# Kernel optimization log

Hardware: AMD Instinct MI355X
Metric: run time of the kernel (lower is better)

The kernel has to match this reference:

```python
import jax, jax.numpy as jnp
import numpy as np
from jax.ops import segment_sum

N_NODES = 10000
N_EDGES = 320000


def leaky_relu(x):
    return jnp.where(x >= 0, x, 0.01 * x)


def gcn_layer(edge_h, src, dst, W, b):
    # (1) node h = mean of incoming edge features
    deg = segment_sum(jnp.ones((edge_h.shape[0],), edge_h.dtype), dst, num_segments=N_NODES)
    deg = jnp.maximum(deg, 1.0)
    h = segment_sum(edge_h, dst, num_segments=N_NODES) / deg[:, None]
    # (2) update_all: node h = sum over in-edges of src node h
    h2 = segment_sum(h[src], dst, num_segments=N_NODES)
    # (3) edge h = mean of endpoint node features
    eh = 0.5 * (h2[src] + h2[dst])
    # (4) linear on edge features
    return eh @ W.T + b


def setup_inputs() -> dict:
    key = jax.random.key(0)
    ks = jax.random.split(key, 20)
    d_in, d_h, d_out = 128, 256, 64
    inp = {
        'inputs1': jax.random.normal(ks[0], (N_EDGES, d_in), jnp.float32),
        'src1': jax.random.randint(ks[1], (N_EDGES,), 0, N_NODES, jnp.int32),
        'dst1': jax.random.randint(ks[2], (N_EDGES,), 0, N_NODES, jnp.int32),
        'inputs2': jax.random.normal(ks[3], (N_EDGES, d_in), jnp.float32),
        'src2': jax.random.randint(ks[4], (N_EDGES,), 0, N_NODES, jnp.int32),
        'dst2': jax.random.randint(ks[5], (N_EDGES,), 0, N_NODES, jnp.int32),
        'W11': jax.random.normal(ks[6], (d_h, d_in), jnp.float32) * 0.05,
        'b11': jax.random.normal(ks[7], (d_h,), jnp.float32) * 0.05,
        'W12': jax.random.normal(ks[8], (d_h, d_h), jnp.float32) * 0.05,
        'b12': jax.random.normal(ks[9], (d_h,), jnp.float32) * 0.05,
        'W21': jax.random.normal(ks[10], (d_h, d_in), jnp.float32) * 0.05,
        'b21': jax.random.normal(ks[11], (d_h,), jnp.float32) * 0.05,
        'W22': jax.random.normal(ks[12], (d_h, d_h), jnp.float32) * 0.05,
        'b22': jax.random.normal(ks[13], (d_h,), jnp.float32) * 0.05,
        'W3': jax.random.normal(ks[14], (d_out, 2 * d_h), jnp.float32) * 0.05,
        'b3': jax.random.normal(ks[15], (d_out,), jnp.float32) * 0.05,
    }
    return inp


def reference(inputs1, src1, dst1, inputs2, src2, dst2,
              W11, b11, W12, b12, W21, b21, W22, b22, W3, b3):
    h1 = leaky_relu(gcn_layer(inputs1, src1, dst1, W11, b11))
    h1 = leaky_relu(gcn_layer(h1, src1, dst1, W12, b12))
    h1 = jnp.mean(h1, axis=0)
    h2 = leaky_relu(gcn_layer(inputs2, src2, dst2, W21, b21))
    h2 = leaky_relu(gcn_layer(h2, src2, dst2, W22, b22))
    h2 = jnp.mean(h2, axis=0)
    out = jnp.concatenate((h1, h2), axis=0)
    return out @ W3.T + b3
```

## Files before the change

### kernel.cpp

```cpp
#include <hip/hip_runtime.h>
#include <cstddef>

#define NN 10000
#define NB 2500

typedef unsigned int u32;
typedef unsigned short u16;
typedef __attribute__((ext_vector_type(8))) short short8;
typedef __attribute__((ext_vector_type(4))) float f32x4;

__device__ __forceinline__ float lrelu(float x) { return x >= 0.f ? x : 0.01f * x; }

__device__ __forceinline__ float bf_lo(u32 v) { union { u32 i; float f; } c; c.i = v << 16; return c.f; }
__device__ __forceinline__ float bf_hi(u32 v) { union { u32 i; float f; } c; c.i = v & 0xFFFF0000u; return c.f; }
__device__ __forceinline__ u32 rne_bits(float f) {
  union { float f; u32 i; } c; c.f = f;
  return c.i + 0x7FFFu + ((c.i >> 16) & 1u);
}
__device__ __forceinline__ u32 pack2(float a, float b) {
  return (rne_bits(a) >> 16) | (rne_bits(b) & 0xFFFF0000u);
}

__global__ __launch_bounds__(256) void wconv_kernel(
    const float* __restrict__ a, const float* __restrict__ b,
    const float* __restrict__ c, const float* __restrict__ d,
    u16* __restrict__ oa, u16* __restrict__ ob,
    u16* __restrict__ oc, u16* __restrict__ od,
    int* __restrict__ degbase ) {
  int i = blockIdx.x * 256 + threadIdx.x;
  if (i < 32768) oa[i] = (u16)(rne_bits(a[i]) >> 16);
  else if (i < 98304) ob[i - 32768] = (u16)(rne_bits(b[i - 32768]) >> 16);
  else if (i < 131072) oc[i - 98304] = (u16)(rne_bits(c[i - 98304]) >> 16);
  else if (i < 196608) od[i - 131072] = (u16)(rne_bits(d[i - 131072]) >> 16);
  if (i < 4 * NN) degbase[i] = 0;
}

__global__ __launch_bounds__(256) void count_b_kernel(const int* __restrict__ dstA,
                                                      const int* __restrict__ dstB,
                                                      int* __restrict__ degbase, int E) {
  const int g = blockIdx.y;
  const int* dst = g ? dstB : dstA;
  int* degi = degbase + (size_t)g * 2 * NN;
  int e = blockIdx.x * 256 + threadIdx.x;
  if (e < E) atomicAdd(&degi[dst[e]], 1);
}

__global__ __launch_bounds__(1024) void scan_b_kernel(const int* __restrict__ degbase,
                                                      int* __restrict__ offbase,
                                                      float* __restrict__ rdegbase, int n) {
  const int g = blockIdx.x;
  const int* degi = degbase + (size_t)g * 2 * NN;
  int* off = offbase + (size_t)g * NN;
  float* rdeg = rdegbase + (size_t)g * NN;
  __shared__ int wsum[16];
  __shared__ int wpre[16];
  __shared__ int carry_s;
  const int tid = threadIdx.x;
  const int lane = tid & 63, w = tid >> 6;
  if (tid == 0) carry_s = 0;
  __syncthreads();
  for (int base = 0; base < n; base += 1024) {
    int i = base + tid;
    int x = (i < n) ? degi[i] : 0;
    int v = x;
#pragma unroll
    for (int d = 1; d < 64; d <<= 1) {
      int t = __shfl_up(v, d);
      if (lane >= d) v += t;
    }
    if (lane == 63) wsum[w] = v;
    __syncthreads();
    if (tid == 0) {
      int s = carry_s;
#pragma unroll
      for (int j = 0; j < 16; ++j) { int t = wsum[j]; wpre[j] = s; s += t; }
      carry_s = s;
    }
    __syncthreads();
    if (i < n) {
      off[i] = wpre[w] + (v - x);
      rdeg[i] = 1.0f / fmaxf((float)x, 1.0f);
    }
    __syncthreads();
  }
}

__global__ __launch_bounds__(256) void fill_b_kernel(const int* __restrict__ srcA,
                                                     const int* __restrict__ dstA,
                                                     const int* __restrict__ srcB,
                                                     const int* __restrict__ dstB,
                                                     const int* __restrict__ offbase,
                                                     int* __restrict__ degbase,
                                                     int* __restrict__ eid_sb,
                                                     int* __restrict__ esrc_sb, int E) {
  const int g = blockIdx.y;
  const int* src = g ? srcB : srcA;
  const int* dst = g ? dstB : dstA;
  const int* off = offbase + (size_t)g * NN;
  int* cursor = degbase + (size_t)g * 2 * NN + NN;
  int* eid_s = eid_sb + (size_t)g * E;
  int* esrc_s = esrc_sb + (size_t)g * E;
  int e = blockIdx.x * 256 + threadIdx.x;
  if (e < E) {
    int d = dst[e];
    int p = off[d] + atomicAdd(&cursor[d], 1);
    eid_s[p] = e;
    esrc_s[p] = src[e];
  }
}

__global__ __launch_bounds__(256) void gatherA_b_kernel(
    const float* __restrict__ featA, const float* __restrict__ featB,
    const int* __restrict__ gidxb, const int* __restrict__ offbase,
    const int* __restrict__ degbase, const float* __restrict__ rdegbase,
    u32* __restrict__ outbfb , int E) {
  const int g = blockIdx.y;
  const float* feat = g ? featB : featA;
  const int* gidx = gidxb + (size_t)g * E;
  const int* off = offbase + (size_t)g * NN;
  const int* degi = degbase + (size_t)g * 2 * NN;
  const float* rdeg = rdegbase + (size_t)g * NN;
  u32* outbf = outbfb + (size_t)g * NN * 64;
  const int n = (blockIdx.x << 2) + (threadIdx.x >> 6);
  const int lane = threadIdx.x & 63;
  const int hl = lane & 31, h = lane >> 5;
  const int o = off[n], d = degi[n];
  const int fo = hl << 2;
  float4 acc = make_float4(0.f, 0.f, 0.f, 0.f);
  for (int c0 = 0; c0 < d; c0 += 64) {
    const int m = min(64, d - c0);
    const int gg = (lane < m) ? gidx[o + c0 + lane] : 0;
    const int pairs = m >> 1;
    int i = 0;
    for (; i + 4 <= pairs; i += 4) {
      const int e0 = 2 * i + h;
      const int s0 = __shfl(gg, e0), s1 = __shfl(gg, e0 + 2);
      const int s2 = __shfl(gg, e0 + 4), s3 = __shfl(gg, e0 + 6);
      const float4 v0 = *(const float4*)&feat[(s0 << 7) + fo];
      const float4 v1 = *(const float4*)&feat[(s1 << 7) + fo];
      const float4 v2 = *(const float4*)&feat[(s2 << 7) + fo];
      const float4 v3 = *(const float4*)&feat[(s3 << 7) + fo];
      acc.x += (v0.x + v1.x) + (v2.x + v3.x);
      acc.y += (v0.y + v1.y) + (v2.y + v3.y);
      acc.z += (v0.z + v1.z) + (v2.z + v3.z);
      acc.w += (v0.w + v1.w) + (v2.w + v3.w);
    }
    for (; i < pairs; ++i) {
      const int s0 = __shfl(gg, 2 * i + h);
      const float4 v0 = *(const float4*)&feat[(s0 << 7) + fo];
      acc.x += v0.x; acc.y += v0.y; acc.z += v0.z; acc.w += v0.w;
    }
    if (m & 1) {
      const int s0 = __shfl(gg, m - 1);
      const float wgt = (h == 0) ? 1.f : 0.f;
      const float4 v0 = *(const float4*)&feat[(s0 << 7) + fo];
      acc.x = fmaf(v0.x, wgt, acc.x);
      acc.y = fmaf(v0.y, wgt, acc.y);
      acc.z = fmaf(v0.z, wgt, acc.z);
      acc.w = fmaf(v0.w, wgt, acc.w);
    }
  }
  acc.x += __shfl(acc.x, lane ^ 32);
  acc.y += __shfl(acc.y, lane ^ 32);
  acc.z += __shfl(acc.z, lane ^ 32);
  acc.w += __shfl(acc.w, lane ^ 32);
  if (h == 0) {
    const float sc = rdeg[n];
    uint2 r;
    r.x = pack2(acc.x * sc, acc.y * sc);
    r.y = pack2(acc.z * sc, acc.w * sc);
    *(uint2*)&outbf[(size_t)n * 64 + (hl << 1)] = r;
  }
}

__global__ __launch_bounds__(256) void gatherB_b_kernel(
    const u32* __restrict__ featb , const int* __restrict__ gidxb,
    const int* __restrict__ offbase, const int* __restrict__ degbase,
    u32* __restrict__ outbfb, int E) {
  const int bid = blockIdx.x;
  const int r = bid & 7, t = bid >> 3;
  const int g = r >> 2;
  const int nb = t * 4 + (r & 3);
  const u32* feat = featb + (size_t)g * NN * 64;
  const int* gidx = gidxb + (size_t)g * E;
  const int* off = offbase + (size_t)g * NN;
  const int* degi = degbase + (size_t)g * 2 * NN;
  u32* outbf = outbfb + (size_t)g * NN * 64;
  const int n = (nb << 2) + (threadIdx.x >> 6);
  const int lane = threadIdx.x & 63;
  const int hl = lane & 31, h = lane >> 5;
  const int o = off[n], d = degi[n];
  const int fo = hl << 1;
  float4 acc = make_float4(0.f, 0.f, 0.f, 0.f);
  for (int c0 = 0; c0 < d; c0 += 64) {
    const int m = min(64, d - c0);
    const int gg = (lane < m) ? gidx[o + c0 + lane] : 0;
    const int pairs = m >> 1;
    int i = 0;
    for (; i + 4 <= pairs; i += 4) {
      const int e0 = 2 * i + h;
      const int s0 = __shfl(gg, e0), s1 = __shfl(gg, e0 + 2);
      const int s2 = __shfl(gg, e0 + 4), s3 = __shfl(gg, e0 + 6);
      const uint2 v0 = *(const uint2*)&feat[(s0 << 6) + fo];
      const uint2 v1 = *(const uint2*)&feat[(s1 << 6) + fo];
      const uint2 v2 = *(const uint2*)&feat[(s2 << 6) + fo];
      const uint2 v3 = *(const uint2*)&feat[(s3 << 6) + fo];
      acc.x += (bf_lo(v0.x) + bf_lo(v1.x)) + (bf_lo(v2.x) + bf_lo(v3.x));
      acc.y += (bf_hi(v0.x) + bf_hi(v1.x)) + (bf_hi(v2.x) + bf_hi(v3.x));
      acc.z += (bf_lo(v0.y) + bf_lo(v1.y)) + (bf_lo(v2.y) + bf_lo(v3.y));
      acc.w += (bf_hi(v0.y) + bf_hi(v1.y)) + (bf_hi(v2.y) + bf_hi(v3.y));
    }
    for (; i < pairs; ++i) {
      const int s0 = __shfl(gg, 2 * i + h);
      const uint2 v0 = *(const uint2*)&feat[(s0 << 6) + fo];
      acc.x += bf_lo(v0.x); acc.y += bf_hi(v0.x);
      acc.z += bf_lo(v0.y); acc.w += bf_hi(v0.y);
    }
    if (m & 1) {
      const int s0 = __shfl(gg, m - 1);
      const float wgt = (h == 0) ? 1.f : 0.f;
      const uint2 v0 = *(const uint2*)&feat[(s0 << 6) + fo];
      acc.x = fmaf(bf_lo(v0.x), wgt, acc.x);
      acc.y = fmaf(bf_hi(v0.x), wgt, acc.y);
      acc.z = fmaf(bf_lo(v0.y), wgt, acc.z);
      acc.w = fmaf(bf_hi(v0.y), wgt, acc.w);
    }
  }
  acc.x += __shfl(acc.x, lane ^ 32);
  acc.y += __shfl(acc.y, lane ^ 32);
  acc.z += __shfl(acc.z, lane ^ 32);
  acc.w += __shfl(acc.w, lane ^ 32);
  if (h == 0) {
    uint2 r2;
    r2.x = pack2(acc.x, acc.y);
    r2.y = pack2(acc.z, acc.w);
    *(uint2*)&outbf[(size_t)n * 64 + (hl << 1)] = r2;
  }
}

__device__ __forceinline__ void acc_bf4(float4& a, uint2 v, const float4& zn, const float4& bb) {
  a.x += lrelu(0.5f * (bf_lo(v.x) + zn.x) + bb.x);
  a.y += lrelu(0.5f * (bf_hi(v.x) + zn.y) + bb.y);
  a.z += lrelu(0.5f * (bf_lo(v.y) + zn.z) + bb.z);
  a.w += lrelu(0.5f * (bf_hi(v.y) + zn.w) + bb.w);
}

__global__ __launch_bounds__(256) void passC_b_kernel(
    const u32* __restrict__ Zb_, const int* __restrict__ esrcb,
    const int* __restrict__ offbase, const int* __restrict__ degbase,
    const float* __restrict__ rdegbase,
    const float* __restrict__ biasA, const float* __restrict__ biasB,
    u32* __restrict__ hBb, int E) {
  const int bid = blockIdx.x;
  const int r = bid & 7, t = bid >> 3;
  const int g = r >> 2, fh = (r >> 1) & 1;
  const int nb = t * 2 + (r & 1);
  const u32* Z = Zb_ + (size_t)g * NN * 128;
  const int* esrc = esrcb + (size_t)g * E;
  const int* off = offbase + (size_t)g * NN;
  const int* degi = degbase + (size_t)g * 2 * NN;
  const float* rdeg = rdegbase + (size_t)g * NN;
  const float* bias = g ? biasB : biasA;
  u32* hB = hBb + (size_t)g * NN * 128;
  const int n = (nb << 2) + (threadIdx.x >> 6);
  const int lane = threadIdx.x & 63;
  const int hl = lane & 31, h = lane >> 5;
  const int o = off[n], d = degi[n];
  const int fo = (fh << 6) + (hl << 1);
  const uint2 znv = *(const uint2*)&Z[(n << 7) + fo];
  const float4 zn = make_float4(bf_lo(znv.x), bf_hi(znv.x), bf_lo(znv.y), bf_hi(znv.y));
  const float4 bb = *(const float4*)&bias[(fh << 7) + (hl << 2)];
  float4 a = make_float4(0.f, 0.f, 0.f, 0.f);
  for (int c0 = 0; c0 < d; c0 += 64) {
    const int m = min(64, d - c0);
    const int gg = (lane < m) ? esrc[o + c0 + lane] : 0;
    const int pairs = m >> 1;
    int i = 0;
    for (; i + 4 <= pairs; i += 4) {
      const int e0 = 2 * i + h;
      const int s0 = __shfl(gg, e0), s1 = __shfl(gg, e0 + 2);
      const int s2 = __shfl(gg, e0 + 4), s3 = __shfl(gg, e0 + 6);
      const uint2 z0 = *(const uint2*)&Z[(s0 << 7) + fo];
      const uint2 z1 = *(const uint2*)&Z[(s1 << 7) + fo];
      const uint2 z2 = *(const uint2*)&Z[(s2 << 7) + fo];
      const uint2 z3 = *(const uint2*)&Z[(s3 << 7) + fo];
      acc_bf4(a, z0, zn, bb);
      acc_bf4(a, z1, zn, bb);
      acc_bf4(a, z2, zn, bb);
      acc_bf4(a, z3, zn, bb);
    }
    for (; i < pairs; ++i) {
      const int s0 = __shfl(gg, 2 * i + h);
      const uint2 z0 = *(const uint2*)&Z[(s0 << 7) + fo];
      acc_bf4(a, z0, zn, bb);
    }
    if (m & 1) {
      const int s0 = __shfl(gg, m - 1);
      const uint2 z0 = *(const uint2*)&Z[(s0 << 7) + fo];
      if (h == 0) acc_bf4(a, z0, zn, bb);
    }
  }
  a.x += __shfl(a.x, lane ^ 32); a.y += __shfl(a.y, lane ^ 32);
  a.z += __shfl(a.z, lane ^ 32); a.w += __shfl(a.w, lane ^ 32);
  if (h == 0) {
    const float rr = rdeg[n];
    uint2 outv;
    outv.x = pack2(a.x * rr, a.y * rr);
    outv.y = pack2(a.z * rr, a.w * rr);
    *(uint2*)&hB[(n << 7) + fo] = outv;
  }
}

__global__ __launch_bounds__(256) void gatherC_b_kernel(
    const u32* __restrict__ featb , const int* __restrict__ gidxb,
    const int* __restrict__ offbase, const int* __restrict__ degbase,
    u32* __restrict__ outbfb, int E) {
  const int bid = blockIdx.x;
  const int r = bid & 7, t = bid >> 3;
  const int g = r >> 2, fh = (r >> 1) & 1;
  const int nb = t * 2 + (r & 1);
  const u32* feat = featb + (size_t)g * NN * 128;
  const int* gidx = gidxb + (size_t)g * E;
  const int* off = offbase + (size_t)g * NN;
  const int* degi = degbase + (size_t)g * 2 * NN;
  u32* outbf = outbfb + (size_t)g * NN * 128;
  const int n = (nb << 2) + (threadIdx.x >> 6);
  const int lane = threadIdx.x & 63;
  const int hl = lane & 31, h = lane >> 5;
  const int o = off[n], d = degi[n];
  const int fo = (fh << 6) + (hl << 1);
  float4 a = make_float4(0.f, 0.f, 0.f, 0.f);
  for (int c0 = 0; c0 < d; c0 += 64) {
    const int m = min(64, d - c0);
    const int gg = (lane < m) ? gidx[o + c0 + lane] : 0;
    const int pairs = m >> 1;
    int i = 0;
    for (; i + 4 <= pairs; i += 4) {
      const int e0 = 2 * i + h;
      const int s0 = __shfl(gg, e0), s1 = __shfl(gg, e0 + 2);
      const int s2 = __shfl(gg, e0 + 4), s3 = __shfl(gg, e0 + 6);
      const uint2 z0 = *(const uint2*)&feat[(s0 << 7) + fo];
      const uint2 z1 = *(const uint2*)&feat[(s1 << 7) + fo];
      const uint2 z2 = *(const uint2*)&feat[(s2 << 7) + fo];
      const uint2 z3 = *(const uint2*)&feat[(s3 << 7) + fo];
      a.x += (bf_lo(z0.x) + bf_lo(z1.x)) + (bf_lo(z2.x) + bf_lo(z3.x));
      a.y += (bf_hi(z0.x) + bf_hi(z1.x)) + (bf_hi(z2.x) + bf_hi(z3.x));
      a.z += (bf_lo(z0.y) + bf_lo(z1.y)) + (bf_lo(z2.y) + bf_lo(z3.y));
      a.w += (bf_hi(z0.y) + bf_hi(z1.y)) + (bf_hi(z2.y) + bf_hi(z3.y));
    }
    for (; i < pairs; ++i) {
      const int s0 = __shfl(gg, 2 * i + h);
      const uint2 z0 = *(const uint2*)&feat[(s0 << 7) + fo];
      a.x += bf_lo(z0.x); a.y += bf_hi(z0.x);
      a.z += bf_lo(z0.y); a.w += bf_hi(z0.y);
    }
    if (m & 1) {
      const int s0 = __shfl(gg, m - 1);
      const uint2 z0 = *(const uint2*)&feat[(s0 << 7) + fo];
      if (h == 0) {
        a.x += bf_lo(z0.x); a.y += bf_hi(z0.x);
        a.z += bf_lo(z0.y); a.w += bf_hi(z0.y);
      }
    }
  }
  a.x += __shfl(a.x, lane ^ 32); a.y += __shfl(a.y, lane ^ 32);
  a.z += __shfl(a.z, lane ^ 32); a.w += __shfl(a.w, lane ^ 32);
  if (h == 0) {
    uint2 outv;
    outv.x = pack2(a.x, a.y);
    outv.y = pack2(a.z, a.w);
    *(uint2*)&outbf[(n << 7) + fo] = outv;
  }
}

__global__ __launch_bounds__(256) void passE_b_kernel(
    const u32* __restrict__ Z2b, const int* __restrict__ esrcb,
    const int* __restrict__ offbase, const int* __restrict__ degbase,
    const float* __restrict__ biasA, const float* __restrict__ biasB,
    float* __restrict__ partialsb , int nNodes, int E) {
  const int bid = blockIdx.x;
  const int r = bid & 7, t = bid >> 3;
  const int g = r >> 2, fh = (r >> 1) & 1;
  const int blk = t * 2 + (r & 1);
  const u32* Z2 = Z2b + (size_t)g * NN * 128;
  const int* esrc = esrcb + (size_t)g * E;
  const int* off = offbase + (size_t)g * NN;
  const int* degi = degbase + (size_t)g * 2 * NN;
  const float* bias = g ? biasB : biasA;
  float* partials = partialsb + (size_t)((g * 2 + fh) * 128 + blk) * 128;
  const int lane = threadIdx.x & 63, w = threadIdx.x >> 6;
  const int hl = lane & 31, h = lane >> 5;
  const int fo = (fh << 6) + (hl << 1);
  const float4 bb = *(const float4*)&bias[(fh << 7) + (hl << 2)];
  float4 a = make_float4(0.f, 0.f, 0.f, 0.f);
  for (int n = blk * 4 + w; n < nNodes; n += 512) {
    const int o = off[n], d = degi[n];
    const uint2 znv = *(const uint2*)&Z2[(n << 7) + fo];
    const float4 zn = make_float4(bf_lo(znv.x), bf_hi(znv.x), bf_lo(znv.y), bf_hi(znv.y));
    for (int c0 = 0; c0 < d; c0 += 64) {
      const int m = min(64, d - c0);
      const int gg = (lane < m) ? esrc[o + c0 + lane] : 0;
      const int pairs = m >> 1;
      int i = 0;
      for (; i + 4 <= pairs; i += 4) {
        const int e0 = 2 * i + h;
        const int s0 = __shfl(gg, e0), s1 = __shfl(gg, e0 + 2);
        const int s2 = __shfl(gg, e0 + 4), s3 = __shfl(gg, e0 + 6);
        const uint2 z0 = *(const uint2*)&Z2[(s0 << 7) + fo];
        const uint2 z1 = *(const uint2*)&Z2[(s1 << 7) + fo];
        const uint2 z2 = *(const uint2*)&Z2[(s2 << 7) + fo];
        const uint2 z3 = *(const uint2*)&Z2[(s3 << 7) + fo];
        acc_bf4(a, z0, zn, bb);
        acc_bf4(a, z1, zn, bb);
        acc_bf4(a, z2, zn, bb);
        acc_bf4(a, z3, zn, bb);
      }
      for (; i < pairs; ++i) {
        const int s0 = __shfl(gg, 2 * i + h);
        const uint2 z0 = *(const uint2*)&Z2[(s0 << 7) + fo];
        acc_bf4(a, z0, zn, bb);
      }
      if (m & 1) {
        const int s0 = __shfl(gg, m - 1);
        const uint2 z0 = *(const uint2*)&Z2[(s0 << 7) + fo];
        if (h == 0) acc_bf4(a, z0, zn, bb);
      }
    }
  }
  a.x += __shfl(a.x, lane ^ 32); a.y += __shfl(a.y, lane ^ 32);
  a.z += __shfl(a.z, lane ^ 32); a.w += __shfl(a.w, lane ^ 32);
  __shared__ float red[4][128];
  if (h == 0) *(float4*)&red[w][hl << 2] = a;
  __syncthreads();
  const int tid = threadIdx.x;
  if (tid < 128) partials[tid] = red[0][tid] + red[1][tid] + red[2][tid] + red[3][tid];
}

__global__ __launch_bounds__(1024) void final_fused_kernel(
    const float* __restrict__ partialsb ,
    const float* __restrict__ W3, const float* __restrict__ b3,
    float* __restrict__ out, float invE) {
  __shared__ float smacc[512];
  __shared__ float tmp2[2][512];
  __shared__ float red[16][64];
  const int tid = threadIdx.x;
  {
    const int half = tid >> 9;
    const int q = tid & 511;
    const float* basep = partialsb + (size_t)(q >> 7) * 128 * 128 + (q & 127);
    float s = 0.f;
    for (int b = half * 64; b < half * 64 + 64; ++b) s += basep[(size_t)b * 128];
    tmp2[half][q] = s;
  }
  __syncthreads();
  if (tid < 512) smacc[tid] = tmp2[0][tid] + tmp2[1][tid];
  __syncthreads();
  const int j = tid & 63, part = tid >> 6;
  float acc = 0.f;
  for (int kk = 0; kk < 32; ++kk) {
    const int k = part * 32 + kk;
    acc += smacc[k] * W3[(size_t)j * 512 + k];
  }
  red[part][j] = acc;
  __syncthreads();
  if (part == 0) {
    float s = 0.f;
#pragma unroll
    for (int p = 0; p < 16; ++p) s += red[p][j];
    out[j] = b3[j] + s * invE;
  }
}

template <int K>
__global__ __launch_bounds__(256) void gemm_mfma_b_kernel(const u16* __restrict__ Ab,
                                                          const u16* __restrict__ WA,
                                                          const u16* __restrict__ WB,
                                                          u16* __restrict__ Cb, int N) {
  const int g = blockIdx.z;
  const u16* A = Ab + (size_t)g * NN * K;
  const u16* Wb = g ? WB : WA;
  u16* C = Cb + (size_t)g * NN * 256;
  const int lane = threadIdx.x & 63;
  const int w = threadIdx.x >> 6;
  const int wm = w >> 1, wn = w & 1;
  const int bn = blockIdx.x * 64 + wm * 32;
  const int bo = blockIdx.y * 64 + wn * 32;
  const int r0 = lane & 15;
  const int kq = lane >> 4;
  const int ra0 = min(bn + r0, N - 1);
  const int ra1 = min(bn + 16 + r0, N - 1);
  const u16* a0p = &A[(size_t)ra0 * K + kq * 8];
  const u16* a1p = &A[(size_t)ra1 * K + kq * 8];
  const u16* b0p = &Wb[(size_t)(bo + r0) * K + kq * 8];
  const u16* b1p = &Wb[(size_t)(bo + 16 + r0) * K + kq * 8];
  f32x4 acc00 = {0.f, 0.f, 0.f, 0.f}, acc01 = {0.f, 0.f, 0.f, 0.f};
  f32x4 acc10 = {0.f, 0.f, 0.f, 0.f}, acc11 = {0.f, 0.f, 0.f, 0.f};
#pragma unroll
  for (int k0 = 0; k0 < K; k0 += 32) {
    const short8 a0 = *(const short8*)(a0p + k0);
    const short8 a1 = *(const short8*)(a1p + k0);
    const short8 b0 = *(const short8*)(b0p + k0);
    const short8 b1 = *(const short8*)(b1p + k0);
    acc00 = __builtin_amdgcn_mfma_f32_16x16x32_bf16(a0, b0, acc00, 0, 0, 0);
    acc01 = __builtin_amdgcn_mfma_f32_16x16x32_bf16(a0, b1, acc01, 0, 0, 0);
    acc10 = __builtin_amdgcn_mfma_f32_16x16x32_bf16(a1, b0, acc10, 0, 0, 0);
    acc11 = __builtin_amdgcn_mfma_f32_16x16x32_bf16(a1, b1, acc11, 0, 0, 0);
  }
#pragma unroll
  for (int r = 0; r < 4; ++r) {
    const int n0 = bn + 4 * kq + r;
    if (n0 < N) {
      C[(size_t)n0 * 256 + bo + r0] = (u16)(rne_bits(acc00[r]) >> 16);
      C[(size_t)n0 * 256 + bo + 16 + r0] = (u16)(rne_bits(acc01[r]) >> 16);
    }
    const int n1 = bn + 16 + 4 * kq + r;
    if (n1 < N) {
      C[(size_t)n1 * 256 + bo + r0] = (u16)(rne_bits(acc10[r]) >> 16);
      C[(size_t)n1 * 256 + bo + 16 + r0] = (u16)(rne_bits(acc11[r]) >> 16);
    }
  }
}

extern "C" void kernel_launch(void* const* d_in, const int* in_sizes, int n_in,
                              void* d_out, int out_size, void* d_ws, size_t ws_size,
                              hipStream_t stream) {
  const float* in1 = (const float*)d_in[0];
  const int* src1 = (const int*)d_in[1];
  const int* dst1 = (const int*)d_in[2];
  const float* in2 = (const float*)d_in[3];
  const int* src2 = (const int*)d_in[4];
  const int* dst2 = (const int*)d_in[5];
  const float* W11 = (const float*)d_in[6];
  const float* b11 = (const float*)d_in[7];
  const float* W12 = (const float*)d_in[8];
  const float* b12 = (const float*)d_in[9];
  const float* W21 = (const float*)d_in[10];
  const float* b21 = (const float*)d_in[11];
  const float* W22 = (const float*)d_in[12];
  const float* b22 = (const float*)d_in[13];
  const float* W3 = (const float*)d_in[14];
  const float* b3 = (const float*)d_in[15];
  const int E = in_sizes[1];
  const int N = NN;

  char* base = (char*)d_ws;
  size_t pos = 0;
  auto carve = [&](size_t bytes) -> char* {
    char* p = base + pos;
    pos = (pos + bytes + 511) & ~(size_t)511;
    return p;
  };
  int* degbase = (int*)carve((size_t)2 * 2 * N * sizeof(int));
  int* offb = (int*)carve((size_t)2 * N * sizeof(int));
  float* rdegb = (float*)carve((size_t)2 * N * sizeof(float));
  int* eid_sb = (int*)carve((size_t)2 * E * sizeof(int));
  int* esrc_sb = (int*)carve((size_t)2 * E * sizeof(int));
  u32* Hb = (u32*)carve((size_t)2 * N * 64 * sizeof(u32));
  u32* H2b = (u32*)carve((size_t)2 * N * 64 * sizeof(u32));
  u32* Zb = (u32*)carve((size_t)2 * N * 128 * sizeof(u32));
  u32* HBb = (u32*)carve((size_t)2 * N * 128 * sizeof(u32));
  u32* H2Bb = (u32*)carve((size_t)2 * N * 128 * sizeof(u32));
  u16* Wa1 = (u16*)carve((size_t)32768 * sizeof(u16));
  u16* Wb1 = (u16*)carve((size_t)65536 * sizeof(u16));
  u16* Wa2 = (u16*)carve((size_t)32768 * sizeof(u16));
  u16* Wb2 = (u16*)carve((size_t)65536 * sizeof(u16));
  float* partialsb = (float*)carve((size_t)2 * 2 * 128 * 128 * sizeof(float));
  (void)ws_size; (void)n_in; (void)out_size;

  const int EB = (E + 255) / 256;
  const dim3 g2(EB, 2);
  const dim3 n2(NB, 2);
  const dim3 gemm_grid((N + 63) / 64, 4, 2);

  wconv_kernel<<<768, 256, 0, stream>>>(W11, W12, W21, W22, Wa1, Wb1, Wa2, Wb2, degbase);

  count_b_kernel<<<g2, 256, 0, stream>>>(dst1, dst2, degbase, E);
  scan_b_kernel<<<2, 1024, 0, stream>>>(degbase, offb, rdegb, N);
  fill_b_kernel<<<g2, 256, 0, stream>>>(src1, dst1, src2, dst2, offb, degbase, eid_sb, esrc_sb, E);

  gatherA_b_kernel<<<n2, 256, 0, stream>>>(in1, in2, eid_sb, offb, degbase, rdegb, Hb, E);
  gatherB_b_kernel<<<2 * NB, 256, 0, stream>>>(Hb, esrc_sb, offb, degbase, H2b, E);
  gemm_mfma_b_kernel<128><<<gemm_grid, 256, 0, stream>>>((const u16*)H2b, Wa1, Wa2, (u16*)Zb, N);

  passC_b_kernel<<<4 * NB, 256, 0, stream>>>(Zb, esrc_sb, offb, degbase, rdegb, b11, b21, HBb, E);
  gatherC_b_kernel<<<4 * NB, 256, 0, stream>>>(HBb, esrc_sb, offb, degbase, H2Bb, E);
  gemm_mfma_b_kernel<256><<<gemm_grid, 256, 0, stream>>>((const u16*)H2Bb, Wb1, Wb2, (u16*)Zb, N);

  passE_b_kernel<<<512, 256, 0, stream>>>(Zb, esrc_sb, offb, degbase, b12, b22, partialsb, N, E);
  final_fused_kernel<<<1, 1024, 0, stream>>>(partialsb, W3, b3, (float*)d_out, 1.0f / (float)E);
}
```

Before: 353.4 us.

## Widen gather loads to 16-byte per lane with quarter-wave edge split

Restructures the four edge-gather kernels so each wavefront splits into four 16-lane groups that each load 8 bf16 features (uint4) per neighbor, instead of two 32-lane halves loading 4 features (uint2). Fewer, wider memory transactions per edge and fewer shuffles per edge-batch are the aim, at the cost of a two-stage cross-lane reduction and more accumulator registers. The leaky-ReLU epilogue is also simplified to fma plus fmax, with the node term and bias precomputed once per node.

Result: faster. 329.7 us (-6.7%).

```diff
diff --git a/kernel.cpp b/kernel.cpp
--- a/kernel.cpp
+++ b/kernel.cpp
@@ -8,8 +8,6 @@
 typedef unsigned short u16;
 typedef __attribute__((ext_vector_type(8))) short short8;
 typedef __attribute__((ext_vector_type(4))) float f32x4;
-
-__device__ __forceinline__ float lrelu(float x) { return x >= 0.f ? x : 0.01f * x; }
 
 __device__ __forceinline__ float bf_lo(u32 v) { union { u32 i; float f; } c; c.i = v << 16; return c.f; }
 __device__ __forceinline__ float bf_hi(u32 v) { union { u32 i; float f; } c; c.i = v & 0xFFFF0000u; return c.f; }
@@ -20,6 +18,7 @@
 __device__ __forceinline__ u32 pack2(float a, float b) {
   return (rne_bits(a) >> 16) | (rne_bits(b) & 0xFFFF0000u);
 }
+__device__ __forceinline__ float lrmax(float x) { return fmaxf(x, 0.01f * x); }
 
 __global__ __launch_bounds__(256) void wconv_kernel(
     const float* __restrict__ a, const float* __restrict__ b,
@@ -173,6 +172,16 @@
   }
 }
 
+#define QREDUCE8(aL, aH)                                                   \
+  aL.x += __shfl(aL.x, lane ^ 16); aL.y += __shfl(aL.y, lane ^ 16);        \
+  aL.z += __shfl(aL.z, lane ^ 16); aL.w += __shfl(aL.w, lane ^ 16);        \
+  aH.x += __shfl(aH.x, lane ^ 16); aH.y += __shfl(aH.y, lane ^ 16);        \
+  aH.z += __shfl(aH.z, lane ^ 16); aH.w += __shfl(aH.w, lane ^ 16);        \
+  aL.x += __shfl(aL.x, lane ^ 32); aL.y += __shfl(aL.y, lane ^ 32);        \
+  aL.z += __shfl(aL.z, lane ^ 32); aL.w += __shfl(aL.w, lane ^ 32);        \
+  aH.x += __shfl(aH.x, lane ^ 32); aH.y += __shfl(aH.y, lane ^ 32);        \
+  aH.z += __shfl(aH.z, lane ^ 32); aH.w += __shfl(aH.w, lane ^ 32);
+
 __global__ __launch_bounds__(256) void gatherB_b_kernel(
     const u32* __restrict__ featb , const int* __restrict__ gidxb,
     const int* __restrict__ offbase, const int* __restrict__ degbase,
@@ -188,61 +197,78 @@
   u32* outbf = outbfb + (size_t)g * NN * 64;
   const int n = (nb << 2) + (threadIdx.x >> 6);
   const int lane = threadIdx.x & 63;
-  const int hl = lane & 31, h = lane >> 5;
+  const int q = lane >> 4, ql = lane & 15;
   const int o = off[n], d = degi[n];
-  const int fo = hl << 1;
-  float4 acc = make_float4(0.f, 0.f, 0.f, 0.f);
+  const int fo = ql << 2;
+  float4 aL = make_float4(0.f, 0.f, 0.f, 0.f), aH = make_float4(0.f, 0.f, 0.f, 0.f);
   for (int c0 = 0; c0 < d; c0 += 64) {
     const int m = min(64, d - c0);
     const int gg = (lane < m) ? gidx[o + c0 + lane] : 0;
-    const int pairs = m >> 1;
+    const int full = m >> 2;
     int i = 0;
-    for (; i + 4 <= pairs; i += 4) {
-      const int e0 = 2 * i + h;
-      const int s0 = __shfl(gg, e0), s1 = __shfl(gg, e0 + 2);
-      const int s2 = __shfl(gg, e0 + 4), s3 = __shfl(gg, e0 + 6);
-      const uint2 v0 = *(const uint2*)&feat[(s0 << 6) + fo];
-      const uint2 v1 = *(const uint2*)&feat[(s1 << 6) + fo];
-      const uint2 v2 = *(const uint2*)&feat[(s2 << 6) + fo];
-      const uint2 v3 = *(const uint2*)&feat[(s3 << 6) + fo];
-      acc.x += (bf_lo(v0.x) + bf_lo(v1.x)) + (bf_lo(v2.x) + bf_lo(v3.x));
-      acc.y += (bf_hi(v0.x) + bf_hi(v1.x)) + (bf_hi(v2.x) + bf_hi(v3.x));
-      acc.z += (bf_lo(v0.y) + bf_lo(v1.y)) + (bf_lo(v2.y) + bf_lo(v3.y));
-      acc.w += (bf_hi(v0.y) + bf_hi(v1.y)) + (bf_hi(v2.y) + bf_hi(v3.y));
-    }
-    for (; i < pairs; ++i) {
-      const int s0 = __shfl(gg, 2 * i + h);
-      const uint2 v0 = *(const uint2*)&feat[(s0 << 6) + fo];
-      acc.x += bf_lo(v0.x); acc.y += bf_hi(v0.x);
-      acc.z += bf_lo(v0.y); acc.w += bf_hi(v0.y);
-    }
-    if (m & 1) {
-      const int s0 = __shfl(gg, m - 1);
-      const float wgt = (h == 0) ? 1.f : 0.f;
-      const uint2 v0 = *(const uint2*)&feat[(s0 << 6) + fo];
-      acc.x = fmaf(bf_lo(v0.x), wgt, acc.x);
-      acc.y = fmaf(bf_hi(v0.x), wgt, acc.y);
-      acc.z = fmaf(bf_lo(v0.y), wgt, acc.z);
-      acc.w = fmaf(bf_hi(v0.y), wgt, acc.w);
-    }
-  }
-  acc.x += __shfl(acc.x, lane ^ 32);
-  acc.y += __shfl(acc.y, lane ^ 32);
-  acc.z += __shfl(acc.z, lane ^ 32);
-  acc.w += __shfl(acc.w, lane ^ 32);
-  if (h == 0) {
-    uint2 r2;
-    r2.x = pack2(acc.x, acc.y);
-    r2.y = pack2(acc.z, acc.w);
-    *(uint2*)&outbf[(size_t)n * 64 + (hl << 1)] = r2;
-  }
-}
-
-__device__ __forceinline__ void acc_bf4(float4& a, uint2 v, const float4& zn, const float4& bb) {
-  a.x += lrelu(0.5f * (bf_lo(v.x) + zn.x) + bb.x);
-  a.y += lrelu(0.5f * (bf_hi(v.x) + zn.y) + bb.y);
-  a.z += lrelu(0.5f * (bf_lo(v.y) + zn.z) + bb.z);
-  a.w += lrelu(0.5f * (bf_hi(v.y) + zn.w) + bb.w);
+    for (; i + 2 <= full; i += 2) {
+      const int e0 = 4 * i + q;
+      const int s0 = __shfl(gg, e0), s1 = __shfl(gg, e0 + 4);
+      const uint4 v0 = *(const uint4*)&feat[(s0 << 6) + fo];
+      const uint4 v1 = *(const uint4*)&feat[(s1 << 6) + fo];
+      aL.x += bf_lo(v0.x) + bf_lo(v1.x); aL.y += bf_hi(v0.x) + bf_hi(v1.x);
+      aL.z += bf_lo(v0.y) + bf_lo(v1.y); aL.w += bf_hi(v0.y) + bf_hi(v1.y);
+      aH.x += bf_lo(v0.z) + bf_lo(v1.z); aH.y += bf_hi(v0.z) + bf_hi(v1.z);
+      aH.z += bf_lo(v0.w) + bf_lo(v1.w); aH.w += bf_hi(v0.w) + bf_hi(v1.w);
+    }
+    if (i < full) {
+      const int s0 = __shfl(gg, 4 * i + q);
+      const uint4 v0 = *(const uint4*)&feat[(s0 << 6) + fo];
+      aL.x += bf_lo(v0.x); aL.y += bf_hi(v0.x);
+      aL.z += bf_lo(v0.y); aL.w += bf_hi(v0.y);
+      aH.x += bf_lo(v0.z); aH.y += bf_hi(v0.z);
+      aH.z += bf_lo(v0.w); aH.w += bf_hi(v0.w);
+    }
+    if (m & 3) {
+      const int e = (m & ~3) + q;
+      const int s0 = __shfl(gg, e < m ? e : (m - 1));
+      const float wgt = (e < m) ? 1.f : 0.f;
+      const uint4 v0 = *(const uint4*)&feat[(s0 << 6) + fo];
+      aL.x = fmaf(bf_lo(v0.x), wgt, aL.x); aL.y = fmaf(bf_hi(v0.x), wgt, aL.y);
+      aL.z = fmaf(bf_lo(v0.y), wgt, aL.z); aL.w = fmaf(bf_hi(v0.y), wgt, aL.w);
+      aH.x = fmaf(bf_lo(v0.z), wgt, aH.x); aH.y = fmaf(bf_hi(v0.z), wgt, aH.y);
+      aH.z = fmaf(bf_lo(v0.w), wgt, aH.z); aH.w = fmaf(bf_hi(v0.w), wgt, aH.w);
+    }
+  }
+  QREDUCE8(aL, aH)
+  if (lane < 16) {
+    uint4 outv;
+    outv.x = pack2(aL.x, aL.y);
+    outv.y = pack2(aL.z, aL.w);
+    outv.z = pack2(aH.x, aH.y);
+    outv.w = pack2(aH.z, aH.w);
+    *(uint4*)&outbf[(n << 6) + fo] = outv;
+  }
+}
+
+__device__ __forceinline__ void acc_lr8(float4& aL, float4& aH, uint4 v,
+                                        const float4& wL, const float4& wH) {
+  float u;
+  u = fmaf(bf_lo(v.x), 0.5f, wL.x); aL.x += lrmax(u);
+  u = fmaf(bf_hi(v.x), 0.5f, wL.y); aL.y += lrmax(u);
+  u = fmaf(bf_lo(v.y), 0.5f, wL.z); aL.z += lrmax(u);
+  u = fmaf(bf_hi(v.y), 0.5f, wL.w); aL.w += lrmax(u);
+  u = fmaf(bf_lo(v.z), 0.5f, wH.x); aH.x += lrmax(u);
+  u = fmaf(bf_hi(v.z), 0.5f, wH.y); aH.y += lrmax(u);
+  u = fmaf(bf_lo(v.w), 0.5f, wH.z); aH.z += lrmax(u);
+  u = fmaf(bf_hi(v.w), 0.5f, wH.w); aH.w += lrmax(u);
+}
+__device__ __forceinline__ void acc_lr8w(float4& aL, float4& aH, uint4 v,
+                                         const float4& wL, const float4& wH, float wgt) {
+  float u;
+  u = fmaf(bf_lo(v.x), 0.5f, wL.x); aL.x = fmaf(lrmax(u), wgt, aL.x);
+  u = fmaf(bf_hi(v.x), 0.5f, wL.y); aL.y = fmaf(lrmax(u), wgt, aL.y);
+  u = fmaf(bf_lo(v.y), 0.5f, wL.z); aL.z = fmaf(lrmax(u), wgt, aL.z);
+  u = fmaf(bf_hi(v.y), 0.5f, wL.w); aL.w = fmaf(lrmax(u), wgt, aL.w);
+  u = fmaf(bf_lo(v.z), 0.5f, wH.x); aH.x = fmaf(lrmax(u), wgt, aH.x);
+  u = fmaf(bf_hi(v.z), 0.5f, wH.y); aH.y = fmaf(lrmax(u), wgt, aH.y);
+  u = fmaf(bf_lo(v.w), 0.5f, wH.z); aH.z = fmaf(lrmax(u), wgt, aH.z);
+  u = fmaf(bf_hi(v.w), 0.5f, wH.w); aH.w = fmaf(lrmax(u), wgt, aH.w);
 }
 
 __global__ __launch_bounds__(256) void passC_b_kernel(
@@ -264,50 +290,53 @@
   u32* hB = hBb + (size_t)g * NN * 128;
   const int n = (nb << 2) + (threadIdx.x >> 6);
   const int lane = threadIdx.x & 63;
-  const int hl = lane & 31, h = lane >> 5;
+  const int q = lane >> 4, ql = lane & 15;
   const int o = off[n], d = degi[n];
-  const int fo = (fh << 6) + (hl << 1);
-  const uint2 znv = *(const uint2*)&Z[(n << 7) + fo];
-  const float4 zn = make_float4(bf_lo(znv.x), bf_hi(znv.x), bf_lo(znv.y), bf_hi(znv.y));
-  const float4 bb = *(const float4*)&bias[(fh << 7) + (hl << 2)];
-  float4 a = make_float4(0.f, 0.f, 0.f, 0.f);
+  const int fo = (fh << 6) + (ql << 2);
+  const uint4 znv = *(const uint4*)&Z[(n << 7) + fo];
+  const float4 bL = *(const float4*)&bias[(fh << 7) + (ql << 3)];
+  const float4 bH = *(const float4*)&bias[(fh << 7) + (ql << 3) + 4];
+  float4 wL, wH;
+  wL.x = fmaf(bf_lo(znv.x), 0.5f, bL.x); wL.y = fmaf(bf_hi(znv.x), 0.5f, bL.y);
+  wL.z = fmaf(bf_lo(znv.y), 0.5f, bL.z); wL.w = fmaf(bf_hi(znv.y), 0.5f, bL.w);
+  wH.x = fmaf(bf_lo(znv.z), 0.5f, bH.x); wH.y = fmaf(bf_hi(znv.z), 0.5f, bH.y);
+  wH.z = fmaf(bf_lo(znv.w), 0.5f, bH.z); wH.w = fmaf(bf_hi(znv.w), 0.5f, bH.w);
+  float4 aL = make_float4(0.f, 0.f, 0.f, 0.f), aH = make_float4(0.f, 0.f, 0.f, 0.f);
   for (int c0 = 0; c0 < d; c0 += 64) {
     const int m = min(64, d - c0);
     const int gg = (lane < m) ? esrc[o + c0 + lane] : 0;
-    const int pairs = m >> 1;
+    const int full = m >> 2;
     int i = 0;
-    for (; i + 4 <= pairs; i += 4) {
-      const int e0 = 2 * i + h;
-      const int s0 = __shfl(gg, e0), s1 = __shfl(gg, e0 + 2);
-      const int s2 = __shfl(gg, e0 + 4), s3 = __shfl(gg, e0 + 6);
-      const uint2 z0 = *(const uint2*)&Z[(s0 << 7) + fo];
-      const uint2 z1 = *(const uint2*)&Z[(s1 << 7) + fo];
-      const uint2 z2 = *(const uint2*)&Z[(s2 << 7) + fo];
-      const uint2 z3 = *(const uint2*)&Z[(s3 << 7) + fo];
-      acc_bf4(a, z0, zn, bb);
-      acc_bf4(a, z1, zn, bb);
-      acc_bf4(a, z2, zn, bb);
-      acc_bf4(a, z3, zn, bb);
-    }
-    for (; i < pairs; ++i) {
-      const int s0 = __shfl(gg, 2 * i + h);
-      const uint2 z0 = *(const uint2*)&Z[(s0 << 7) + fo];
-      acc_bf4(a, z0, zn, bb);
-    }
-    if (m & 1) {
-      const int s0 = __shfl(gg, m - 1);
-      const uint2 z0 = *(const uint2*)&Z[(s0 << 7) + fo];
-      if (h == 0) acc_bf4(a, z0, zn, bb);
-    }
-  }
-  a.x += __shfl(a.x, lane ^ 32); a.y += __shfl(a.y, lane ^ 32);
-  a.z += __shfl(a.z, lane ^ 32); a.w += __shfl(a.w, lane ^ 32);
-  if (h == 0) {
+    for (; i + 2 <= full; i += 2) {
+      const int e0 = 4 * i + q;
+      const int s0 = __shfl(gg, e0), s1 = __shfl(gg, e0 + 4);
+      const uint4 z0 = *(const uint4*)&Z[(s0 << 7) + fo];
+      const uint4 z1 = *(const uint4*)&Z[(s1 << 7) + fo];
+      acc_lr8(aL, aH, z0, wL, wH);
+      acc_lr8(aL, aH, z1, wL, wH);
+    }
+    if (i < full) {
+      const int s0 = __shfl(gg, 4 * i + q);
+      const uint4 z0 = *(const uint4*)&Z[(s0 << 7) + fo];
+      acc_lr8(aL, aH, z0, wL, wH);
+    }
+    if (m & 3) {
+      const int e = (m & ~3) + q;
+      const int s0 = __shfl(gg, e < m ? e : (m - 1));
+      const float wgt = (e < m) ? 1.f : 0.f;
+      const uint4 z0 = *(const uint4*)&Z[(s0 << 7) + fo];
+      acc_lr8w(aL, aH, z0, wL, wH, wgt);
+    }
+  }
+  QREDUCE8(aL, aH)
+  if (lane < 16) {
     const float rr = rdeg[n];
-    uint2 outv;
-    outv.x = pack2(a.x * rr, a.y * rr);
-    outv.y = pack2(a.z * rr, a.w * rr);
-    *(uint2*)&hB[(n << 7) + fo] = outv;
+    uint4 outv;
+    outv.x = pack2(aL.x * rr, aL.y * rr);
+    outv.y = pack2(aL.z * rr, aL.w * rr);
+    outv.z = pack2(aH.x * rr, aH.y * rr);
+    outv.w = pack2(aH.z * rr, aH.w * rr);
+    *(uint4*)&hB[(n << 7) + fo] = outv;
   }
 }
 
@@ -326,50 +355,52 @@
   u32* outbf = outbfb + (size_t)g * NN * 128;
   const int n = (nb << 2) + (threadIdx.x >> 6);
   const int lane = threadIdx.x & 63;
-  const int hl = lane & 31, h = lane >> 5;
+  const int q = lane >> 4, ql = lane & 15;
   const int o = off[n], d = degi[n];
-  const int fo = (fh << 6) + (hl << 1);
-  float4 a = make_float4(0.f, 0.f, 0.f, 0.f);
+  const int fo = (fh << 6) + (ql << 2);
+  float4 aL = make_float4(0.f, 0.f, 0.f, 0.f), aH = make_float4(0.f, 0.f, 0.f, 0.f);
   for (int c0 = 0; c0 < d; c0 += 64) {
     const int m = min(64, d - c0);
     const int gg = (lane < m) ? gidx[o + c0 + lane] : 0;
-    const int pairs = m >> 1;
+    const int full = m >> 2;
     int i = 0;
-    for (; i + 4 <= pairs; i += 4) {
-      const int e0 = 2 * i + h;
-      const int s0 = __shfl(gg, e0), s1 = __shfl(gg, e0 + 2);
-      const int s2 = __shfl(gg, e0 + 4), s3 = __shfl(gg, e0 + 6);
-      const uint2 z0 = *(const uint2*)&feat[(s0 << 7) + fo];
-      const uint2 z1 = *(const uint2*)&feat[(s1 << 7) + fo];
-      const uint2 z2 = *(const uint2*)&feat[(s2 << 7) + fo];
-      const uint2 z3 = *(const uint2*)&feat[(s3 << 7) + fo];
-      a.x += (bf_lo(z0.x) + bf_lo(z1.x)) + (bf_lo(z2.x) + bf_lo(z3.x));
-      a.y += (bf_hi(z0.x) + bf_hi(z1.x)) + (bf_hi(z2.x) + bf_hi(z3.x));
-      a.z += (bf_lo(z0.y) + bf_lo(z1.y)) + (bf_lo(z2.y) + bf_lo(z3.y));
-      a.w += (bf_hi(z0.y) + bf_hi(z1.y)) + (bf_hi(z2.y) + bf_hi(z3.y));
-    }
-    for (; i < pairs; ++i) {
-      const int s0 = __shfl(gg, 2 * i + h);
-      const uint2 z0 = *(const uint2*)&feat[(s0 << 7) + fo];
-      a.x += bf_lo(z0.x); a.y += bf_hi(z0.x);
-      a.z += bf_lo(z0.y); a.w += bf_hi(z0.y);
-    }
-    if (m & 1) {
-      const int s0 = __shfl(gg, m - 1);
-      const uint2 z0 = *(const uint2*)&feat[(s0 << 7) + fo];
-      if (h == 0) {
-        a.x += bf_lo(z0.x); a.y += bf_hi(z0.x);
-        a.z += bf_lo(z0.y); a.w += bf_hi(z0.y);
-      }
-    }
-  }
-  a.x += __shfl(a.x, lane ^ 32); a.y += __shfl(a.y, lane ^ 32);
-  a.z += __shfl(a.z, lane ^ 32); a.w += __shfl(a.w, lane ^ 32);
-  if (h == 0) {
-    uint2 outv;
-    outv.x = pack2(a.x, a.y);
-    outv.y = pack2(a.z, a.w);
-    *(uint2*)&outbf[(n << 7) + fo] = outv;
+    for (; i + 2 <= full; i += 2) {
+      const int e0 = 4 * i + q;
+      const int s0 = __shfl(gg, e0), s1 = __shfl(gg, e0 + 4);
+      const uint4 z0 = *(const uint4*)&feat[(s0 << 7) + fo];
+      const uint4 z1 = *(const uint4*)&feat[(s1 << 7) + fo];
+      aL.x += bf_lo(z0.x) + bf_lo(z1.x); aL.y += bf_hi(z0.x) + bf_hi(z1.x);
+      aL.z += bf_lo(z0.y) + bf_lo(z1.y); aL.w += bf_hi(z0.y) + bf_hi(z1.y);
+      aH.x += bf_lo(z0.z) + bf_lo(z1.z); aH.y += bf_hi(z0.z) + bf_hi(z1.z);
+      aH.z += bf_lo(z0.w) + bf_lo(z1.w); aH.w += bf_hi(z0.w) + bf_hi(z1.w);
+    }
+    if (i < full) {
+      const int s0 = __shfl(gg, 4 * i + q);
+      const uint4 z0 = *(const uint4*)&feat[(s0 << 7) + fo];
+      aL.x += bf_lo(z0.x); aL.y += bf_hi(z0.x);
+      aL.z += bf_lo(z0.y); aL.w += bf_hi(z0.y);
+      aH.x += bf_lo(z0.z); aH.y += bf_hi(z0.z);
+      aH.z += bf_lo(z0.w); aH.w += bf_hi(z0.w);
+    }
+    if (m & 3) {
+      const int e = (m & ~3) + q;
+      const int s0 = __shfl(gg, e < m ? e : (m - 1));
+      const float wgt = (e < m) ? 1.f : 0.f;
+      const uint4 z0 = *(const uint4*)&feat[(s0 << 7) + fo];
+      aL.x = fmaf(bf_lo(z0.x), wgt, aL.x); aL.y = fmaf(bf_hi(z0.x), wgt, aL.y);
+      aL.z = fmaf(bf_lo(z0.y), wgt, aL.z); aL.w = fmaf(bf_hi(z0.y), wgt, aL.w);
+      aH.x = fmaf(bf_lo(z0.z), wgt, aH.x); aH.y = fmaf(bf_hi(z0.z), wgt, aH.y);
+      aH.z = fmaf(bf_lo(z0.w), wgt, aH.z); aH.w = fmaf(bf_hi(z0.w), wgt, aH.w);
+    }
+  }
+  QREDUCE8(aL, aH)
+  if (lane < 16) {
+    uint4 outv;
+    outv.x = pack2(aL.x, aL.y);
+    outv.y = pack2(aL.z, aL.w);
+    outv.z = pack2(aH.x, aH.y);
+    outv.w = pack2(aH.z, aH.w);
+    *(uint4*)&outbf[(n << 7) + fo] = outv;
   }
 }
 
@@ -389,48 +420,52 @@
   const float* bias = g ? biasB : biasA;
   float* partials = partialsb + (size_t)((g * 2 + fh) * 128 + blk) * 128;
   const int lane = threadIdx.x & 63, w = threadIdx.x >> 6;
-  const int hl = lane & 31, h = lane >> 5;
-  const int fo = (fh << 6) + (hl << 1);
-  const float4 bb = *(const float4*)&bias[(fh << 7) + (hl << 2)];
-  float4 a = make_float4(0.f, 0.f, 0.f, 0.f);
+  const int q = lane >> 4, ql = lane & 15;
+  const int fo = (fh << 6) + (ql << 2);
+  const float4 bL = *(const float4*)&bias[(fh << 7) + (ql << 3)];
+  const float4 bH = *(const float4*)&bias[(fh << 7) + (ql << 3) + 4];
+  float4 aL = make_float4(0.f, 0.f, 0.f, 0.f), aH = make_float4(0.f, 0.f, 0.f, 0.f);
   for (int n = blk * 4 + w; n < nNodes; n += 512) {
     const int o = off[n], d = degi[n];
-    const uint2 znv = *(const uint2*)&Z2[(n << 7) + fo];
-    const float4 zn = make_float4(bf_lo(znv.x), bf_hi(znv.x), bf_lo(znv.y), bf_hi(znv.y));
+    const uint4 znv = *(const uint4*)&Z2[(n << 7) + fo];
+    float4 wL, wH;
+    wL.x = fmaf(bf_lo(znv.x), 0.5f, bL.x); wL.y = fmaf(bf_hi(znv.x), 0.5f, bL.y);
+    wL.z = fmaf(bf_lo(znv.y), 0.5f, bL.z); wL.w = fmaf(bf_hi(znv.y), 0.5f, bL.w);
+    wH.x = fmaf(bf_lo(znv.z), 0.5f, bH.x); wH.y = fmaf(bf_hi(znv.z), 0.5f, bH.y);
+    wH.z = fmaf(bf_lo(znv.w), 0.5f, bH.z); wH.w = fmaf(bf_hi(znv.w), 0.5f, bH.w);
     for (int c0 = 0; c0 < d; c0 += 64) {
       const int m = min(64, d - c0);
       const int gg = (lane < m) ? esrc[o + c0 + lane] : 0;
-      const int pairs = m >> 1;
+      const int full = m >> 2;
       int i = 0;
-      for (; i + 4 <= pairs; i += 4) {
-        const int e0 = 2 * i + h;
-        const int s0 = __shfl(gg, e0), s1 = __shfl(gg, e0 + 2);
-        const int s2 = __shfl(gg, e0 + 4), s3 = __shfl(gg, e0 + 6);
-        const uint2 z0 = *(const uint2*)&Z2[(s0 << 7) + fo];
-        const uint2 z1 = *(const uint2*)&Z2[(s1 << 7) + fo];
-        const uint2 z2 = *(const uint2*)&Z2[(s2 << 7) + fo];
-        const uint2 z3 = *(const uint2*)&Z2[(s3 << 7) + fo];
-        acc_bf4(a, z0, zn, bb);
-        acc_bf4(a, z1, zn, bb);
-        acc_bf4(a, z2, zn, bb);
-        acc_bf4(a, z3, zn, bb);
+      for (; i + 2 <= full; i += 2) {
+        const int e0 = 4 * i + q;
+        const int s0 = __shfl(gg, e0), s1 = __shfl(gg, e0 + 4);
+        const uint4 z0 = *(const uint4*)&Z2[(s0 << 7) + fo];
+        const uint4 z1 = *(const uint4*)&Z2[(s1 << 7) + fo];
+        acc_lr8(aL, aH, z0, wL, wH);
+        acc_lr8(aL, aH, z1, wL, wH);
       }
-      for (; i < pairs; ++i) {
-        const int s0 = __shfl(gg, 2 * i + h);
-        const uint2 z0 = *(const uint2*)&Z2[(s0 << 7) + fo];
-        acc_bf4(a, z0, zn, bb);
+      if (i < full) {
+        const int s0 = __shfl(gg, 4 * i + q);
+        const uint4 z0 = *(const uint4*)&Z2[(s0 << 7) + fo];
+        acc_lr8(aL, aH, z0, wL, wH);
       }
-      if (m & 1) {
-        const int s0 = __shfl(gg, m - 1);
-        const uint2 z0 = *(const uint2*)&Z2[(s0 << 7) + fo];
-        if (h == 0) acc_bf4(a, z0, zn, bb);
+      if (m & 3) {
+        const int e = (m & ~3) + q;
+        const int s0 = __shfl(gg, e < m ? e : (m - 1));
+        const float wgt = (e < m) ? 1.f : 0.f;
+        const uint4 z0 = *(const uint4*)&Z2[(s0 << 7) + fo];
+        acc_lr8w(aL, aH, z0, wL, wH, wgt);
       }
     }
   }
-  a.x += __shfl(a.x, lane ^ 32); a.y += __shfl(a.y, lane ^ 32);
-  a.z += __shfl(a.z, lane ^ 32); a.w += __shfl(a.w, lane ^ 32);
+  QREDUCE8(aL, aH)
   __shared__ float red[4][128];
-  if (h == 0) *(float4*)&red[w][hl << 2] = a;
+  if (lane < 16) {
+    *(float4*)&red[w][ql << 3] = aL;
+    *(float4*)&red[w][(ql << 3) + 4] = aH;
+  }
   __syncthreads();
   const int tid = threadIdx.x;
   if (tid < 128) partials[tid] = red[0][tid] + red[1][tid] + red[2][tid] + red[3][tid];
```
